# Kernel tuning notes

Measured on AMD Instinct MI355X. Metric: run time of the kernel, lower is better.

Reference implementation:

```python
import jax, jax.numpy as jnp
import numpy as np

N = 25000      # nodes
E = 400000     # edges (before self loops)
G = 64         # graphs in batch
H = 16         # attention heads
ITER = 10      # stacked main GATv2 layers


def setup_inputs():
    key = jax.random.key(0)
    c = [0]
    def nk():
        c[0] += 1
        return jax.random.fold_in(key, c[0])
    def glorot(shape):
        fan = shape[-2] + shape[-1]
        return jax.random.normal(nk(), shape, jnp.float32) * np.float32(np.sqrt(2.0 / fan))
    inp = {
        "x": jax.random.normal(nk(), (N, 2), jnp.float32),
        "edge_attr": jax.random.normal(nk(), (E, 2), jnp.float32),
        "edge_index": jax.random.randint(nk(), (2, E), 0, N, jnp.int32),
        "mask": jax.random.randint(nk(), (N,), 0, 2, jnp.int32),
        "batch": jnp.sort(jax.random.randint(nk(), (N,), 0, G, jnp.int32)),
        # gcn: GATv2Conv(2, 4, heads=16, edge_dim=2), concat -> 64
        "g0_Wl": glorot((2, 64)), "g0_bl": jnp.zeros((64,), jnp.float32),
        "g0_Wr": glorot((2, 64)), "g0_br": jnp.zeros((64,), jnp.float32),
        "g0_We": glorot((2, 64)), "g0_att": glorot((H, 4)),
        "g0_bias": jnp.zeros((64,), jnp.float32),
        "bn_gamma": jnp.ones((64,), jnp.float32),
        "bn_beta": jnp.zeros((64,), jnp.float32),
        "m_Wl": glorot((ITER, 64, 64)), "m_bl": jnp.zeros((ITER, 64), jnp.float32),
        "m_Wr": glorot((ITER, 64, 64)), "m_br": jnp.zeros((ITER, 64), jnp.float32),
        "m_We": glorot((ITER, 2, 64)), "m_att": glorot((ITER, H, 4)),
        "m_bias": jnp.zeros((ITER, 64), jnp.float32),
        # final: GATv2Conv(64, 1, heads=16, concat=False)
        "f_Wl": glorot((64, 16)), "f_bl": jnp.zeros((16,), jnp.float32),
        "f_Wr": glorot((64, 16)), "f_br": jnp.zeros((16,), jnp.float32),
        "f_We": glorot((2, 16)), "f_att": glorot((H, 1)),
        "f_bias": jnp.zeros((1,), jnp.float32),
        # sbs: GATv2Conv(64, 1, heads=16, concat=False)
        "s_Wl": glorot((64, 16)), "s_bl": jnp.zeros((16,), jnp.float32),
        "s_Wr": glorot((64, 16)), "s_br": jnp.zeros((16,), jnp.float32),
        "s_We": glorot((2, 16)), "s_att": glorot((H, 1)),
        "s_bias": jnp.zeros((1,), jnp.float32),
    }
    return inp


def _gatv2(x, src, dst, eattr, Wl, bl, Wr, br, We, att, bias, concat):
    """PyG GATv2Conv: x_l[j]+x_r[i]+e -> LeakyReLU(0.2) -> att dot -> segment softmax over dst."""
    n = x.shape[0]
    h, c = att.shape
    xl = (x @ Wl + bl).reshape(n, h, c)
    xr = (x @ Wr + br).reshape(n, h, c)
    e = (eattr @ We).reshape(-1, h, c)
    m = jax.nn.leaky_relu(xl[src] + xr[dst] + e, 0.2)          # [Etot,H,C]
    logit = jnp.einsum('ehc,hc->eh', m, att)                    # [Etot,H]
    lmax = jax.ops.segment_max(logit, dst, num_segments=n)
    ex = jnp.exp(logit - lmax[dst])
    den = jax.ops.segment_sum(ex, dst, num_segments=n)
    alpha = ex / den[dst]
    out = jax.ops.segment_sum(xl[src] * alpha[..., None], dst, num_segments=n)  # [N,H,C]
    out = out.reshape(n, h * c) if concat else out.mean(axis=1)
    return out + bias


def reference(x, edge_attr, edge_index, mask, batch,
              g0_Wl, g0_bl, g0_Wr, g0_br, g0_We, g0_att, g0_bias,
              bn_gamma, bn_beta,
              m_Wl, m_bl, m_Wr, m_br, m_We, m_att, m_bias,
              f_Wl, f_bl, f_Wr, f_br, f_We, f_att, f_bias,
              s_Wl, s_bl, s_Wr, s_br, s_We, s_att, s_bias):
    n = x.shape[0]
    src, dst = edge_index[0], edge_index[1]
    # add self loops; self-loop edge attr = mean of incoming edge attrs (fill_value='mean')
    ones = jnp.ones((src.shape[0],), jnp.float32)
    cnt = jax.ops.segment_sum(ones, dst, num_segments=n)
    esum = jax.ops.segment_sum(edge_attr, dst, num_segments=n)
    loop_attr = esum / jnp.maximum(cnt, 1.0)[:, None]
    arng = jnp.arange(n, dtype=edge_index.dtype)
    src2 = jnp.concatenate([src, arng])
    dst2 = jnp.concatenate([dst, arng])
    ea2 = jnp.concatenate([edge_attr, loop_attr], axis=0)

    h0 = _gatv2(x, src2, dst2, ea2, g0_Wl, g0_bl, g0_Wr, g0_br, g0_We, g0_att, g0_bias, True)
    mu = h0.mean(axis=0)
    var = h0.var(axis=0)
    h = jax.nn.leaky_relu((h0 - mu) * jax.lax.rsqrt(var + 1e-5) * bn_gamma + bn_beta, 0.01)

    def step(hc, p):
        Wl, bl, Wr, br, We, att, bias = p
        hc = jax.nn.leaky_relu(_gatv2(hc, src2, dst2, ea2, Wl, bl, Wr, br, We, att, bias, True), 0.01)
        return hc, None
    h, _ = jax.lax.scan(step, h, (m_Wl, m_bl, m_Wr, m_br, m_We, m_att, m_bias))

    mus = _gatv2(h, src2, dst2, ea2, s_Wl, s_bl, s_Wr, s_br, s_We, s_att, s_bias, False)[:, 0]  # [N]
    fin = _gatv2(h, src2, dst2, ea2, f_Wl, f_bl, f_Wr, f_br, f_We, f_att, f_bias, False)        # [N,1]
    w = (mask == 0).astype(jnp.float32)
    sums = jax.ops.segment_sum(fin * w[:, None], batch, num_segments=G)
    cnts = jax.ops.segment_sum(w, batch, num_segments=G)
    sat = (sums / jnp.maximum(cnts, 1.0)[:, None])[:, 0]  # [G]
    return mus, sat
```

## Files before the change

### kernel.cpp

```cpp
#include <hip/hip_runtime.h>


static __device__ __forceinline__ float lrelu(float x, float s) {
    return fmaxf(x, s * x);
}

__global__ void k_build0(const int* __restrict__ dst, int* __restrict__ cnt,
                         int* __restrict__ rank, int E) {
    int idx = blockIdx.x * blockDim.x + threadIdx.x;
    if (idx < E) rank[idx] = atomicAdd(&cnt[dst[idx]], 1);
}

__global__ void k_segoff(const int* __restrict__ cnt, int* __restrict__ row_start,
                         int* __restrict__ cursor, int n) {
    int i = blockIdx.x * blockDim.x + threadIdx.x;
    int lane = threadIdx.x & 63;
    int v = (i < n) ? cnt[i] : 0;
    int s = v;
#pragma unroll
    for (int off = 1; off < 64; off <<= 1) {
        int t = __shfl_up(s, off);
        if (lane >= off) s += t;
    }
    int wavetot = __shfl(s, 63);
    int base = 0;
    if (lane == 63) base = atomicAdd(cursor, wavetot);
    base = __shfl(base, 63);
    if (i < n) row_start[i] = base + s - v;
}

__global__ void k_scatter(const int* __restrict__ src, const int* __restrict__ dst,
                          const float* __restrict__ ea, const int* __restrict__ rank,
                          const int* __restrict__ row_start,
                          int* __restrict__ csr_src, float* __restrict__ csr_ea, int E) {
    int e = blockIdx.x * blockDim.x + threadIdx.x;
    if (e >= E) return;
    int pos = row_start[dst[e]] + rank[e];
    csr_src[pos] = src[e];
    *(float2*)(csr_ea + 2 * (size_t)pos) = *(const float2*)(ea + 2 * (size_t)e);
}

__launch_bounds__(256, 8)
__global__ void k_gat0(const float* __restrict__ x,
                       const int* __restrict__ row_start, const int* __restrict__ cnt,
                       const int* __restrict__ csr_src, const float* __restrict__ csr_ea,
                       const float* __restrict__ Wl, const float* __restrict__ bl,
                       const float* __restrict__ Wr, const float* __restrict__ br,
                       const float* __restrict__ We, const float* __restrict__ att,
                       const float* __restrict__ bias,
                       float* __restrict__ out, int n) {
    int d = (blockIdx.x * blockDim.x + threadIdx.x) >> 6;
    int lane = threadIdx.x & 63;
    if (d >= n) return;
    const int p0 = __builtin_amdgcn_readfirstlane(row_start[d]);
    const int deg = __builtin_amdgcn_readfirstlane(cnt[d]);
    const int p1 = p0 + deg;
    const float wl0 = Wl[lane], wl1 = Wl[64 + lane], blv = bl[lane];
    const float we0 = We[lane], we1 = We[64 + lane];
    const float av = att[lane];
    const float2 xd = *(const float2*)(x + 2 * (size_t)d);
    const float xrv = fmaf(xd.x, Wr[lane], fmaf(xd.y, Wr[64 + lane], br[lane]));

    float den0 = 0.f, acc0 = 0.f;
    float den1 = 0.f, acc1 = 0.f;
    float s0 = 0.f, s1 = 0.f;

    auto step = [&](float xv, float2 ea, bool valid, float& den, float& acc) {
        float vm = valid ? 1.f : 0.f;
        s0 = fmaf(vm, ea.x, s0);
        s1 = fmaf(vm, ea.y, s1);
        float tv = lrelu(xv + xrv + ea.x * we0 + ea.y * we1, 0.2f) * av;
        tv += __shfl_xor(tv, 1);
        tv += __shfl_xor(tv, 2);
        if (!valid) tv = -__builtin_inff();
        float w = __expf(tv);
        den += w;
        acc += w * xv;
    };

    for (int p = p0; p < p1; p += 4) {
        int q1 = min(p + 1, p1 - 1), q2 = min(p + 2, p1 - 1), q3 = min(p + 3, p1 - 1);
        int e0s = csr_src[p], e1s = csr_src[q1], e2s = csr_src[q2], e3s = csr_src[q3];
        float2 ea0 = *(const float2*)(csr_ea + 2 * (size_t)p);
        float2 ea1 = *(const float2*)(csr_ea + 2 * (size_t)q1);
        float2 ea2 = *(const float2*)(csr_ea + 2 * (size_t)q2);
        float2 ea3 = *(const float2*)(csr_ea + 2 * (size_t)q3);
        float2 xs0 = *(const float2*)(x + 2 * (size_t)e0s);
        float2 xs1 = *(const float2*)(x + 2 * (size_t)e1s);
        float2 xs2 = *(const float2*)(x + 2 * (size_t)e2s);
        float2 xs3 = *(const float2*)(x + 2 * (size_t)e3s);
        float xv0 = fmaf(xs0.x, wl0, fmaf(xs0.y, wl1, blv));
        float xv1 = fmaf(xs1.x, wl0, fmaf(xs1.y, wl1, blv));
        float xv2 = fmaf(xs2.x, wl0, fmaf(xs2.y, wl1, blv));
        float xv3 = fmaf(xs3.x, wl0, fmaf(xs3.y, wl1, blv));
        step(xv0, ea0, true, den0, acc0);
        step(xv1, ea1, p + 1 < p1, den1, acc1);
        step(xv2, ea2, p + 2 < p1, den0, acc0);
        step(xv3, ea3, p + 3 < p1, den1, acc1);
    }
    {
        float c = fmaxf((float)deg, 1.f);
        float se0 = s0 / c, se1 = s1 / c;
        float xv = fmaf(xd.x, wl0, fmaf(xd.y, wl1, blv));
        float tv = lrelu(xv + xrv + se0 * we0 + se1 * we1, 0.2f) * av;
        tv += __shfl_xor(tv, 1);
        tv += __shfl_xor(tv, 2);
        float w = __expf(tv);
        den0 += w;
        acc0 += w * xv;
    }
    out[((size_t)d << 6) + lane] = (acc0 + acc1) / (den0 + den1) + bias[lane];
}

__launch_bounds__(256)
__global__ void k_proj64(const float* __restrict__ h,
                         const float* __restrict__ Wl, const float* __restrict__ bl,
                         const float* __restrict__ Wr, const float* __restrict__ br,
                         const double* __restrict__ stats,
                         const float* __restrict__ bng, const float* __restrict__ bnb,
                         float* __restrict__ xl, float* __restrict__ xr, int n) {
    __shared__ float wsl[4096], wsr[4096], bna[64], bnbb[64];
    int t = threadIdx.x;
    for (int i = t; i < 4096; i += 256) { wsl[i] = Wl[i]; wsr[i] = Wr[i]; }
    if (t < 64) {
        double mu = stats[t] / n;
        double var = stats[64 + t] / n - mu * mu;
        float rs = (float)(1.0 / sqrt(var + 1e-5));
        float a = rs * bng[t];
        bna[t] = a;
        bnbb[t] = bnb[t] - (float)mu * a;
    }
    __syncthreads();
    int rg = t >> 2, cg4 = (t & 3) << 4;
    int r0 = blockIdx.x * 128 + rg * 2;
    float accl[2][16], accr[2][16];
#pragma unroll
    for (int r = 0; r < 2; ++r)
#pragma unroll
        for (int j = 0; j < 16; ++j) { accl[r][j] = 0.f; accr[r][j] = 0.f; }
    for (int k0 = 0; k0 < 64; k0 += 4) {
        float hk[2][4];
#pragma unroll
        for (int r = 0; r < 2; ++r) {
            int gr = r0 + r;
            float4 v = (gr < n) ? *(const float4*)(h + (size_t)gr * 64 + k0)
                                : make_float4(0.f, 0.f, 0.f, 0.f);
            hk[r][0] = v.x; hk[r][1] = v.y; hk[r][2] = v.z; hk[r][3] = v.w;
#pragma unroll
            for (int kk = 0; kk < 4; ++kk)
                hk[r][kk] = lrelu(hk[r][kk] * bna[k0 + kk] + bnbb[k0 + kk], 0.01f);
        }
#pragma unroll
        for (int kk = 0; kk < 4; ++kk) {
            const float* wl = wsl + (k0 + kk) * 64 + cg4;
            const float* wr = wsr + (k0 + kk) * 64 + cg4;
#pragma unroll
            for (int r = 0; r < 2; ++r)
#pragma unroll
                for (int j = 0; j < 16; ++j) {
                    accl[r][j] += hk[r][kk] * wl[j];
                    accr[r][j] += hk[r][kk] * wr[j];
                }
        }
    }
#pragma unroll
    for (int r = 0; r < 2; ++r) {
        int gr = r0 + r;
        if (gr < n) {
            float* ol = xl + (size_t)gr * 64 + cg4;
            float* orr = xr + (size_t)gr * 64 + cg4;
#pragma unroll
            for (int j = 0; j < 16; ++j) {
                ol[j] = accl[r][j] + bl[cg4 + j];
                orr[j] = accr[r][j] + br[cg4 + j];
            }
        }
    }
}

__device__ __forceinline__ float gat_node(const float* __restrict__ xl,
                                          const float* __restrict__ xr,
                                          const int* __restrict__ row_start,
                                          const int* __restrict__ cnt,
                                          const int* __restrict__ csr_src,
                                          const float* __restrict__ csr_ea,
                                          const float* __restrict__ We,
                                          const float* __restrict__ att,
                                          const float* __restrict__ bias,
                                          int d, int lane, int relu) {
    const int p0 = __builtin_amdgcn_readfirstlane(row_start[d]);
    const int deg = __builtin_amdgcn_readfirstlane(cnt[d]);
    const int p1 = p0 + deg;
    const float we0 = We[lane], we1 = We[64 + lane];
    const float av = att[lane];
    const float xrv = xr[((size_t)d << 6) + lane];

    float den0 = 0.f, acc0 = 0.f;
    float den1 = 0.f, acc1 = 0.f;
    float s0 = 0.f, s1 = 0.f;

    auto step = [&](float xv, float2 ea, bool valid, float& den, float& acc) {
        float vm = valid ? 1.f : 0.f;
        s0 = fmaf(vm, ea.x, s0);
        s1 = fmaf(vm, ea.y, s1);
        float tv = lrelu(xv + xrv + ea.x * we0 + ea.y * we1, 0.2f) * av;
        tv += __shfl_xor(tv, 1);
        tv += __shfl_xor(tv, 2);
        if (!valid) tv = -__builtin_inff();
        float w = __expf(tv);
        den += w;
        acc += w * xv;
    };

    for (int p = p0; p < p1; p += 4) {
        int q1 = min(p + 1, p1 - 1), q2 = min(p + 2, p1 - 1), q3 = min(p + 3, p1 - 1);
        int e0s = csr_src[p], e1s = csr_src[q1], e2s = csr_src[q2], e3s = csr_src[q3];
        float2 e0 = *(const float2*)(csr_ea + 2 * (size_t)p);
        float2 e1 = *(const float2*)(csr_ea + 2 * (size_t)q1);
        float2 e2 = *(const float2*)(csr_ea + 2 * (size_t)q2);
        float2 e3 = *(const float2*)(csr_ea + 2 * (size_t)q3);
        float x0 = xl[((size_t)e0s << 6) + lane];
        float x1 = xl[((size_t)e1s << 6) + lane];
        float x2 = xl[((size_t)e2s << 6) + lane];
        float x3 = xl[((size_t)e3s << 6) + lane];
        step(x0, e0, true, den0, acc0);
        step(x1, e1, p + 1 < p1, den1, acc1);
        step(x2, e2, p + 2 < p1, den0, acc0);
        step(x3, e3, p + 3 < p1, den1, acc1);
    }
    {
        float c = fmaxf((float)deg, 1.f);
        float se0 = s0 / c, se1 = s1 / c;
        float xv = xl[((size_t)d << 6) + lane];
        float tv = lrelu(xv + xrv + se0 * we0 + se1 * we1, 0.2f) * av;
        tv += __shfl_xor(tv, 1);
        tv += __shfl_xor(tv, 2);
        float w = __expf(tv);
        den0 += w;
        acc0 += w * xv;
    }
    float o = (acc0 + acc1) / (den0 + den1) + bias[lane];
    if (relu) o = lrelu(o, 0.01f);
    return o;
}

__launch_bounds__(64, 8)
__global__ void k_gat_proj2(const float* __restrict__ xl, const float* __restrict__ xr,
                            const int* __restrict__ row_start, const int* __restrict__ cnt,
                            const int* __restrict__ csr_src, const float* __restrict__ csr_ea,
                            const float* __restrict__ We, const float* __restrict__ att,
                            const float* __restrict__ bias,
                            const float* __restrict__ Wnl, const float* __restrict__ bnl,
                            const float* __restrict__ Wnr, const float* __restrict__ bnr,
                            float* __restrict__ xl_out, float* __restrict__ xr_out, int n) {
    int wave = blockIdx.x;
    int lane = threadIdx.x & 63;
    int d0 = wave * 2, d1 = d0 + 1;
    if (d0 >= n) return;
    float o0 = gat_node(xl, xr, row_start, cnt, csr_src, csr_ea, We, att, bias, d0, lane, 1);
    float o1 = (d1 < n)
                   ? gat_node(xl, xr, row_start, cnt, csr_src, csr_ea, We, att, bias, d1, lane, 1)
                   : 0.f;
    float al0a = 0.f, al0b = 0.f, ar0a = 0.f, ar0b = 0.f;
    float al1a = 0.f, al1b = 0.f, ar1a = 0.f, ar1b = 0.f;
#pragma unroll 4
    for (int k = 0; k < 64; k += 2) {
        float h0a = __shfl(o0, k), h0b = __shfl(o0, k + 1);
        float h1a = __shfl(o1, k), h1b = __shfl(o1, k + 1);
        float wl0 = Wnl[k * 64 + lane], wl1 = Wnl[(k + 1) * 64 + lane];
        float wr0 = Wnr[k * 64 + lane], wr1 = Wnr[(k + 1) * 64 + lane];
        al0a += h0a * wl0; al0b += h0b * wl1;
        ar0a += h0a * wr0; ar0b += h0b * wr1;
        al1a += h1a * wl0; al1b += h1b * wl1;
        ar1a += h1a * wr0; ar1b += h1b * wr1;
    }
    float bL = bnl[lane], bR = bnr[lane];
    xl_out[((size_t)d0 << 6) + lane] = al0a + al0b + bL;
    xr_out[((size_t)d0 << 6) + lane] = ar0a + ar0b + bR;
    if (d1 < n) {
        xl_out[((size_t)d1 << 6) + lane] = al1a + al1b + bL;
        xr_out[((size_t)d1 << 6) + lane] = ar1a + ar1b + bR;
    }
}

__launch_bounds__(64, 8)
__global__ void k_gat_projfin2(const float* __restrict__ xl, const float* __restrict__ xr,
                               const int* __restrict__ row_start, const int* __restrict__ cnt,
                               const int* __restrict__ csr_src, const float* __restrict__ csr_ea,
                               const float* __restrict__ We, const float* __restrict__ att,
                               const float* __restrict__ bias,
                               const float* __restrict__ fWl, const float* __restrict__ fbl,
                               const float* __restrict__ fWr, const float* __restrict__ fbr,
                               const float* __restrict__ sWl, const float* __restrict__ sbl,
                               const float* __restrict__ sWr, const float* __restrict__ sbr,
                               float* __restrict__ packed, int n) {
    int wave = blockIdx.x;
    int lane = threadIdx.x & 63;
    int d0 = wave * 2, d1 = d0 + 1;
    if (d0 >= n) return;
    float o0 = gat_node(xl, xr, row_start, cnt, csr_src, csr_ea, We, att, bias, d0, lane, 1);
    float o1 = (d1 < n)
                   ? gat_node(xl, xr, row_start, cnt, csr_src, csr_ea, We, att, bias, d1, lane, 1)
                   : 0.f;
    int q = lane >> 4, cc = lane & 15;
    const float* W = (q == 0) ? fWl : (q == 1) ? sWl : (q == 2) ? fWr : sWr;
    const float* B = (q == 0) ? fbl : (q == 1) ? sbl : (q == 2) ? fbr : sbr;
    float a0 = 0.f, a1 = 0.f, b0 = 0.f, b1 = 0.f;
#pragma unroll 4
    for (int k = 0; k < 64; k += 2) {
        float w0 = W[k * 16 + cc], w1 = W[(k + 1) * 16 + cc];
        a0 += __shfl(o0, k) * w0;
        a1 += __shfl(o0, k + 1) * w1;
        b0 += __shfl(o1, k) * w0;
        b1 += __shfl(o1, k + 1) * w1;
    }
    float bb = B[cc];
    packed[((size_t)d0 << 6) + lane] = a0 + a1 + bb;
    if (d1 < n) packed[((size_t)d1 << 6) + lane] = b0 + b1 + bb;
}

__launch_bounds__(256)
__global__ void k_gat_final(const float* __restrict__ packed,
                            const int* __restrict__ row_start, const int* __restrict__ cnt,
                            const int* __restrict__ csr_src, const float* __restrict__ csr_ea,
                            const float* __restrict__ fWe, const float* __restrict__ sWe,
                            const float* __restrict__ fatt, const float* __restrict__ satt,
                            const float* __restrict__ fbias, const float* __restrict__ sbias,
                            float* __restrict__ fin, float* __restrict__ mus, int n) {
    int hw = (blockIdx.x * blockDim.x + threadIdx.x) >> 5;
    if (hw >= n) return;
    int l = threadIdx.x & 31;
    int hh = l & 15, sel = l >> 4;
    const int d = hw;
    const int p0 = row_start[d], deg = cnt[d], p1 = p0 + deg;
    const float* We = sel ? sWe : fWe;
    float we0 = We[hh], we1 = We[16 + hh];
    float av = (sel ? satt : fatt)[hh];
    float xrv = packed[(size_t)d * 64 + 32 + sel * 16 + hh];
    int xli = sel * 16 + hh;

    float den0 = 0.f, acc0 = 0.f;
    float den1 = 0.f, acc1 = 0.f;
    float s0 = 0.f, s1 = 0.f;

    auto step = [&](float xv, float2 ea, bool valid, float& den, float& acc) {
        float vm = valid ? 1.f : 0.f;
        s0 = fmaf(vm, ea.x, s0);
        s1 = fmaf(vm, ea.y, s1);
        float t = lrelu(xv + xrv + ea.x * we0 + ea.y * we1, 0.2f) * av;
        if (!valid) t = -__builtin_inff();
        float w = __expf(t);
        den += w;
        acc += w * xv;
    };

    for (int p = p0; p < p1; p += 4) {
        int q1 = min(p + 1, p1 - 1), q2 = min(p + 2, p1 - 1), q3 = min(p + 3, p1 - 1);
        int e0s = csr_src[p], e1s = csr_src[q1], e2s = csr_src[q2], e3s = csr_src[q3];
        float2 e0 = *(const float2*)(csr_ea + 2 * (size_t)p);
        float2 e1 = *(const float2*)(csr_ea + 2 * (size_t)q1);
        float2 e2 = *(const float2*)(csr_ea + 2 * (size_t)q2);
        float2 e3 = *(const float2*)(csr_ea + 2 * (size_t)q3);
        float x0 = packed[(size_t)e0s * 64 + xli];
        float x1 = packed[(size_t)e1s * 64 + xli];
        float x2 = packed[(size_t)e2s * 64 + xli];
        float x3 = packed[(size_t)e3s * 64 + xli];
        step(x0, e0, true, den0, acc0);
        step(x1, e1, p + 1 < p1, den1, acc1);
        step(x2, e2, p + 2 < p1, den0, acc0);
        step(x3, e3, p + 3 < p1, den1, acc1);
    }
    {
        float c = fmaxf((float)deg, 1.f);
        float se0 = s0 / c, se1 = s1 / c;
        float xv = packed[(size_t)d * 64 + xli];
        float t = lrelu(xv + xrv + se0 * we0 + se1 * we1, 0.2f) * av;
        float w = __expf(t);
        den0 += w;
        acc0 += w * xv;
    }
    float val = (acc0 + acc1) / (den0 + den1);
#pragma unroll
    for (int w = 1; w < 16; w <<= 1) val += __shfl_xor(val, w);
    if ((threadIdx.x & 15) == 0) {
        float o = val * (1.f / 16.f) + (sel ? sbias[0] : fbias[0]);
        if (sel) mus[d] = o; else fin[d] = o;
    }
}


__global__ void k_bnstats(const float* __restrict__ h, double* __restrict__ stats, int n) {
    int c = threadIdx.x & 63;
    int s0 = blockIdx.x * (blockDim.x >> 6) + (threadIdx.x >> 6);
    int ns = gridDim.x * (blockDim.x >> 6);
    double s = 0.0, s2 = 0.0;
    for (int i = s0; i < n; i += ns) {
        float v = h[(size_t)i * 64 + c];
        s += v;
        s2 += (double)v * v;
    }
    atomicAdd(&stats[c], s);
    atomicAdd(&stats[64 + c], s2);
}


__global__ void k_sat_acc(const float* __restrict__ fin, const int* __restrict__ mask,
                          const int* __restrict__ batch,
                          float* __restrict__ sums, float* __restrict__ cnts, int n) {
    int i = blockIdx.x * blockDim.x + threadIdx.x;
    int lane = threadIdx.x & 63;
    int g = (i < n) ? batch[i] : -1;
    float c = (i < n && mask[i] == 0) ? 1.f : 0.f;
    float v = (c > 0.f) ? fin[i] : 0.f;
#pragma unroll
    for (int off = 1; off < 64; off <<= 1) {
        float v2 = __shfl_down(v, off);
        float c2 = __shfl_down(c, off);
        int g2 = __shfl_down(g, off);
        if (lane + off < 64 && g2 == g) { v += v2; c += c2; }
    }
    int gprev = __shfl_up(g, 1);
    bool head = (lane == 0) || (gprev != g);
    if (head && g >= 0 && c > 0.f) {
        atomicAdd(&sums[g], v);
        atomicAdd(&cnts[g], c);
    }
}

__global__ void k_sat_fin(const float* __restrict__ sums, const float* __restrict__ cnts,
                          float* __restrict__ out, int g) {
    int i = threadIdx.x;
    if (i < g) out[i] = sums[i] / fmaxf(cnts[i], 1.f);
}


extern "C" void kernel_launch(void* const* d_in, const int* in_sizes, int n_in,
                              void* d_out, int out_size, void* d_ws, size_t ws_size,
                              hipStream_t stream) {
    const float* x = (const float*)d_in[0];
    const float* eat = (const float*)d_in[1];
    const int* ei = (const int*)d_in[2];
    const int* mask = (const int*)d_in[3];
    const int* batch = (const int*)d_in[4];
    const float* g0_Wl = (const float*)d_in[5];
    const float* g0_bl = (const float*)d_in[6];
    const float* g0_Wr = (const float*)d_in[7];
    const float* g0_br = (const float*)d_in[8];
    const float* g0_We = (const float*)d_in[9];
    const float* g0_att = (const float*)d_in[10];
    const float* g0_bias = (const float*)d_in[11];
    const float* bn_g = (const float*)d_in[12];
    const float* bn_b = (const float*)d_in[13];
    const float* m_Wl = (const float*)d_in[14];
    const float* m_bl = (const float*)d_in[15];
    const float* m_Wr = (const float*)d_in[16];
    const float* m_br = (const float*)d_in[17];
    const float* m_We = (const float*)d_in[18];
    const float* m_att = (const float*)d_in[19];
    const float* m_bias = (const float*)d_in[20];
    const float* f_Wl = (const float*)d_in[21];
    const float* f_bl = (const float*)d_in[22];
    const float* f_Wr = (const float*)d_in[23];
    const float* f_br = (const float*)d_in[24];
    const float* f_We = (const float*)d_in[25];
    const float* f_att = (const float*)d_in[26];
    const float* f_bias = (const float*)d_in[27];
    const float* s_Wl = (const float*)d_in[28];
    const float* s_bl = (const float*)d_in[29];
    const float* s_Wr = (const float*)d_in[30];
    const float* s_br = (const float*)d_in[31];
    const float* s_We = (const float*)d_in[32];
    const float* s_att = (const float*)d_in[33];
    const float* s_bias = (const float*)d_in[34];

    const int N = in_sizes[3];
    const int E = in_sizes[1] / 2;
    const int G = out_size - N;
    const int ITER = in_sizes[14] / 4096;
    const int* srcp = ei;
    const int* dstp = ei + E;

    char* wsb = (char*)d_ws;
    size_t off = 0;
    auto alloc = [&](size_t b) { void* p = wsb + off; off = (off + b + 255) & ~(size_t)255; return p; };
    int* cnt = (int*)alloc((size_t)N * 4);
    int* cursor = (int*)alloc(256);
    double* stats = (double*)alloc(128 * 8);
    float* sums = (float*)alloc((size_t)G * 4);
    float* cnts = (float*)alloc((size_t)G * 4);
    size_t zero_bytes = off;
    int* rank = (int*)alloc((size_t)E * 4);
    int* row_start = (int*)alloc((size_t)N * 4);
    int* csr_src = (int*)alloc((size_t)(E + 4) * 4);
    float* csr_ea = (float*)alloc((size_t)(E + 4) * 8);
    float* xlA = (float*)alloc((size_t)N * 256);
    float* xrA = (float*)alloc((size_t)N * 256);
    float* xlB = (float*)alloc((size_t)N * 256);
    float* xrB = (float*)alloc((size_t)N * 256);
    float* hbuf = (float*)alloc((size_t)N * 256);
    float* fin = (float*)alloc((size_t)N * 4);
    (void)ws_size; (void)n_in;

    float* outv = (float*)d_out;

    hipMemsetAsync(d_ws, 0, zero_bytes, stream);
    const int tb = 256;
    const int ggrid = (N * 64 + 255) / 256;
    const int npair = (N + 1) / 2;
    k_build0<<<(E + tb - 1) / tb, tb, 0, stream>>>(dstp, cnt, rank, E);
    k_segoff<<<(N + tb - 1) / tb, tb, 0, stream>>>(cnt, row_start, cursor, N);
    k_scatter<<<(E + tb - 1) / tb, tb, 0, stream>>>(srcp, dstp, eat, rank, row_start,
                                                    csr_src, csr_ea, E);

    k_gat0<<<ggrid, tb, 0, stream>>>(x, row_start, cnt, csr_src, csr_ea,
                                     g0_Wl, g0_bl, g0_Wr, g0_br,
                                     g0_We, g0_att, g0_bias, hbuf, N);
    k_bnstats<<<128, 256, 0, stream>>>(hbuf, stats, N);
    k_proj64<<<(N + 127) / 128, 256, 0, stream>>>(hbuf, m_Wl, m_bl, m_Wr, m_br,
                                                  stats, bn_g, bn_b, xlA, xrA, N);

    float* cur_l = xlA; float* cur_r = xrA;
    float* alt_l = xlB; float* alt_r = xrB;
    for (int l = 0; l < ITER; ++l) {
        if (l < ITER - 1) {
            k_gat_proj2<<<npair, 64, 0, stream>>>(cur_l, cur_r, row_start, cnt, csr_src, csr_ea,
                                                  m_We + l * 128, m_att + l * 64, m_bias + l * 64,
                                                  m_Wl + (size_t)(l + 1) * 4096, m_bl + (l + 1) * 64,
                                                  m_Wr + (size_t)(l + 1) * 4096, m_br + (l + 1) * 64,
                                                  alt_l, alt_r, N);
        } else {
            k_gat_projfin2<<<npair, 64, 0, stream>>>(cur_l, cur_r, row_start, cnt, csr_src, csr_ea,
                                                     m_We + l * 128, m_att + l * 64, m_bias + l * 64,
                                                     f_Wl, f_bl, f_Wr, f_br,
                                                     s_Wl, s_bl, s_Wr, s_br,
                                                     alt_l, N);
        }
        float* t;
        t = cur_l; cur_l = alt_l; alt_l = t;
        t = cur_r; cur_r = alt_r; alt_r = t;
    }
    k_gat_final<<<(N * 32 + tb - 1) / tb, tb, 0, stream>>>(cur_l, row_start, cnt, csr_src, csr_ea,
                                                           f_We, s_We, f_att, s_att,
                                                           f_bias, s_bias, fin, outv, N);
    k_sat_acc<<<(N + tb - 1) / tb, tb, 0, stream>>>(fin, mask, batch, sums, cnts, N);
    k_sat_fin<<<1, 64, 0, stream>>>(sums, cnts, outv + N, G);
}
```

Measured before the change: 627.3 us.

## Split fused GAT aggregation and projection into separate kernels with LDS-tiled GEMM

Unfuses each main layer into a pure aggregation kernel (256-thread blocks, two nodes per wave, writing h to a buffer) and a separate projection kernel that stages the 64x64 weights in shared memory and computes a register-tiled 2x16 output per thread. The old fused path read weights from global memory per wave and used many shuffles. The new path removes that cost and lets the aggregation run at higher occupancy. In exchange it adds an extra write and read of the N x 64 hidden state plus an extra kernel launch per layer.

```diff
diff --git a/kernel.cpp b/kernel.cpp
--- a/kernel.cpp
+++ b/kernel.cpp
@@ -244,79 +244,133 @@
     return o;
 }
 
-__launch_bounds__(64, 8)
-__global__ void k_gat_proj2(const float* __restrict__ xl, const float* __restrict__ xr,
-                            const int* __restrict__ row_start, const int* __restrict__ cnt,
-                            const int* __restrict__ csr_src, const float* __restrict__ csr_ea,
-                            const float* __restrict__ We, const float* __restrict__ att,
-                            const float* __restrict__ bias,
-                            const float* __restrict__ Wnl, const float* __restrict__ bnl,
-                            const float* __restrict__ Wnr, const float* __restrict__ bnr,
-                            float* __restrict__ xl_out, float* __restrict__ xr_out, int n) {
-    int wave = blockIdx.x;
+__launch_bounds__(256, 8)
+__global__ void k_gat2e(const float* __restrict__ xl, const float* __restrict__ xr,
+                        const int* __restrict__ row_start, const int* __restrict__ cnt,
+                        const int* __restrict__ csr_src, const float* __restrict__ csr_ea,
+                        const float* __restrict__ We, const float* __restrict__ att,
+                        const float* __restrict__ bias,
+                        float* __restrict__ out, int n) {
+    int wave = (blockIdx.x * blockDim.x + threadIdx.x) >> 6;
     int lane = threadIdx.x & 63;
-    int d0 = wave * 2, d1 = d0 + 1;
+    int d0 = wave * 2;
     if (d0 >= n) return;
     float o0 = gat_node(xl, xr, row_start, cnt, csr_src, csr_ea, We, att, bias, d0, lane, 1);
-    float o1 = (d1 < n)
-                   ? gat_node(xl, xr, row_start, cnt, csr_src, csr_ea, We, att, bias, d1, lane, 1)
-                   : 0.f;
-    float al0a = 0.f, al0b = 0.f, ar0a = 0.f, ar0b = 0.f;
-    float al1a = 0.f, al1b = 0.f, ar1a = 0.f, ar1b = 0.f;
-#pragma unroll 4
-    for (int k = 0; k < 64; k += 2) {
-        float h0a = __shfl(o0, k), h0b = __shfl(o0, k + 1);
-        float h1a = __shfl(o1, k), h1b = __shfl(o1, k + 1);
-        float wl0 = Wnl[k * 64 + lane], wl1 = Wnl[(k + 1) * 64 + lane];
-        float wr0 = Wnr[k * 64 + lane], wr1 = Wnr[(k + 1) * 64 + lane];
-        al0a += h0a * wl0; al0b += h0b * wl1;
-        ar0a += h0a * wr0; ar0b += h0b * wr1;
-        al1a += h1a * wl0; al1b += h1b * wl1;
-        ar1a += h1a * wr0; ar1b += h1b * wr1;
-    }
-    float bL = bnl[lane], bR = bnr[lane];
-    xl_out[((size_t)d0 << 6) + lane] = al0a + al0b + bL;
-    xr_out[((size_t)d0 << 6) + lane] = ar0a + ar0b + bR;
+    out[((size_t)d0 << 6) + lane] = o0;
+    int d1 = d0 + 1;
     if (d1 < n) {
-        xl_out[((size_t)d1 << 6) + lane] = al1a + al1b + bL;
-        xr_out[((size_t)d1 << 6) + lane] = ar1a + ar1b + bR;
-    }
-}
-
-__launch_bounds__(64, 8)
-__global__ void k_gat_projfin2(const float* __restrict__ xl, const float* __restrict__ xr,
-                               const int* __restrict__ row_start, const int* __restrict__ cnt,
-                               const int* __restrict__ csr_src, const float* __restrict__ csr_ea,
-                               const float* __restrict__ We, const float* __restrict__ att,
-                               const float* __restrict__ bias,
-                               const float* __restrict__ fWl, const float* __restrict__ fbl,
-                               const float* __restrict__ fWr, const float* __restrict__ fbr,
-                               const float* __restrict__ sWl, const float* __restrict__ sbl,
-                               const float* __restrict__ sWr, const float* __restrict__ sbr,
-                               float* __restrict__ packed, int n) {
-    int wave = blockIdx.x;
-    int lane = threadIdx.x & 63;
-    int d0 = wave * 2, d1 = d0 + 1;
-    if (d0 >= n) return;
-    float o0 = gat_node(xl, xr, row_start, cnt, csr_src, csr_ea, We, att, bias, d0, lane, 1);
-    float o1 = (d1 < n)
-                   ? gat_node(xl, xr, row_start, cnt, csr_src, csr_ea, We, att, bias, d1, lane, 1)
-                   : 0.f;
-    int q = lane >> 4, cc = lane & 15;
-    const float* W = (q == 0) ? fWl : (q == 1) ? sWl : (q == 2) ? fWr : sWr;
-    const float* B = (q == 0) ? fbl : (q == 1) ? sbl : (q == 2) ? fbr : sbr;
-    float a0 = 0.f, a1 = 0.f, b0 = 0.f, b1 = 0.f;
-#pragma unroll 4
-    for (int k = 0; k < 64; k += 2) {
-        float w0 = W[k * 16 + cc], w1 = W[(k + 1) * 16 + cc];
-        a0 += __shfl(o0, k) * w0;
-        a1 += __shfl(o0, k + 1) * w1;
-        b0 += __shfl(o1, k) * w0;
-        b1 += __shfl(o1, k + 1) * w1;
-    }
-    float bb = B[cc];
-    packed[((size_t)d0 << 6) + lane] = a0 + a1 + bb;
-    if (d1 < n) packed[((size_t)d1 << 6) + lane] = b0 + b1 + bb;
+        float o1 = gat_node(xl, xr, row_start, cnt, csr_src, csr_ea, We, att, bias, d1, lane, 1);
+        out[((size_t)d1 << 6) + lane] = o1;
+    }
+}
+
+__launch_bounds__(256)
+__global__ void k_projdual(const float* __restrict__ h,
+                           const float* __restrict__ Wl, const float* __restrict__ bl,
+                           const float* __restrict__ Wr, const float* __restrict__ br,
+                           float* __restrict__ xl, float* __restrict__ xr, int n) {
+    __shared__ float wsl[4096], wsr[4096];
+    int t = threadIdx.x;
+    for (int i = t; i < 4096; i += 256) { wsl[i] = Wl[i]; wsr[i] = Wr[i]; }
+    __syncthreads();
+    int rg = t >> 2, cg4 = (t & 3) << 4;
+    int r0 = blockIdx.x * 128 + rg * 2;
+    float accl[2][16], accr[2][16];
+#pragma unroll
+    for (int r = 0; r < 2; ++r)
+#pragma unroll
+        for (int j = 0; j < 16; ++j) { accl[r][j] = 0.f; accr[r][j] = 0.f; }
+    for (int k0 = 0; k0 < 64; k0 += 4) {
+        float hk[2][4];
+#pragma unroll
+        for (int r = 0; r < 2; ++r) {
+            int gr = r0 + r;
+            float4 v = (gr < n) ? *(const float4*)(h + (size_t)gr * 64 + k0)
+                                : make_float4(0.f, 0.f, 0.f, 0.f);
+            hk[r][0] = v.x; hk[r][1] = v.y; hk[r][2] = v.z; hk[r][3] = v.w;
+        }
+#pragma unroll
+        for (int kk = 0; kk < 4; ++kk) {
+            const float* wl = wsl + (k0 + kk) * 64 + cg4;
+            const float* wr = wsr + (k0 + kk) * 64 + cg4;
+#pragma unroll
+            for (int r = 0; r < 2; ++r)
+#pragma unroll
+                for (int j = 0; j < 16; ++j) {
+                    accl[r][j] += hk[r][kk] * wl[j];
+                    accr[r][j] += hk[r][kk] * wr[j];
+                }
+        }
+    }
+#pragma unroll
+    for (int r = 0; r < 2; ++r) {
+        int gr = r0 + r;
+        if (gr < n) {
+            float* ol = xl + (size_t)gr * 64 + cg4;
+            float* orr = xr + (size_t)gr * 64 + cg4;
+#pragma unroll
+            for (int j = 0; j < 16; ++j) {
+                ol[j] = accl[r][j] + bl[cg4 + j];
+                orr[j] = accr[r][j] + br[cg4 + j];
+            }
+        }
+    }
+}
+
+__launch_bounds__(256)
+__global__ void k_projpk(const float* __restrict__ h,
+                         const float* __restrict__ fWl, const float* __restrict__ fbl,
+                         const float* __restrict__ sWl, const float* __restrict__ sbl,
+                         const float* __restrict__ fWr, const float* __restrict__ fbr,
+                         const float* __restrict__ sWr, const float* __restrict__ sbr,
+                         float* __restrict__ packed, int n) {
+    __shared__ float ws[4096], bs[64];
+    int t = threadIdx.x;
+    for (int i = t; i < 4096; i += 256) {
+        int k = i >> 6, c = i & 63, q = c >> 4, cc = c & 15;
+        const float* W = (q == 0) ? fWl : (q == 1) ? sWl : (q == 2) ? fWr : sWr;
+        ws[i] = W[k * 16 + cc];
+    }
+    if (t < 64) {
+        int q = t >> 4, cc = t & 15;
+        const float* B = (q == 0) ? fbl : (q == 1) ? sbl : (q == 2) ? fbr : sbr;
+        bs[t] = B[cc];
+    }
+    __syncthreads();
+    int rg = t >> 2, cg4 = (t & 3) << 4;
+    int r0 = blockIdx.x * 128 + rg * 2;
+    float acc[2][16];
+#pragma unroll
+    for (int r = 0; r < 2; ++r)
+#pragma unroll
+        for (int j = 0; j < 16; ++j) acc[r][j] = 0.f;
+    for (int k0 = 0; k0 < 64; k0 += 4) {
+        float hk[2][4];
+#pragma unroll
+        for (int r = 0; r < 2; ++r) {
+            int gr = r0 + r;
+            float4 v = (gr < n) ? *(const float4*)(h + (size_t)gr * 64 + k0)
+                                : make_float4(0.f, 0.f, 0.f, 0.f);
+            hk[r][0] = v.x; hk[r][1] = v.y; hk[r][2] = v.z; hk[r][3] = v.w;
+        }
+#pragma unroll
+        for (int kk = 0; kk < 4; ++kk) {
+            const float* w = ws + (k0 + kk) * 64 + cg4;
+#pragma unroll
+            for (int r = 0; r < 2; ++r)
+#pragma unroll
+                for (int j = 0; j < 16; ++j) acc[r][j] += hk[r][kk] * w[j];
+        }
+    }
+#pragma unroll
+    for (int r = 0; r < 2; ++r) {
+        int gr = r0 + r;
+        if (gr < n) {
+            float* op = packed + (size_t)gr * 64 + cg4;
+#pragma unroll
+            for (int j = 0; j < 16; ++j) op[j] = acc[r][j] + bs[cg4 + j];
+        }
+    }
 }
 
 __launch_bounds__(256)
@@ -507,6 +561,8 @@
     const int tb = 256;
     const int ggrid = (N * 64 + 255) / 256;
     const int npair = (N + 1) / 2;
+    const int ggrid2 = (npair * 64 + 255) / 256;
+    const int pgrid = (N + 127) / 128;
     k_build0<<<(E + tb - 1) / tb, tb, 0, stream>>>(dstp, cnt, rank, E);
     k_segoff<<<(N + tb - 1) / tb, tb, 0, stream>>>(cnt, row_start, cursor, N);
     k_scatter<<<(E + tb - 1) / tb, tb, 0, stream>>>(srcp, dstp, eat, rank, row_start,
@@ -516,24 +572,25 @@
                                      g0_Wl, g0_bl, g0_Wr, g0_br,
                                      g0_We, g0_att, g0_bias, hbuf, N);
     k_bnstats<<<128, 256, 0, stream>>>(hbuf, stats, N);
-    k_proj64<<<(N + 127) / 128, 256, 0, stream>>>(hbuf, m_Wl, m_bl, m_Wr, m_br,
-                                                  stats, bn_g, bn_b, xlA, xrA, N);
+    k_proj64<<<pgrid, 256, 0, stream>>>(hbuf, m_Wl, m_bl, m_Wr, m_br,
+                                        stats, bn_g, bn_b, xlA, xrA, N);
 
     float* cur_l = xlA; float* cur_r = xrA;
     float* alt_l = xlB; float* alt_r = xrB;
     for (int l = 0; l < ITER; ++l) {
+        k_gat2e<<<ggrid2, tb, 0, stream>>>(cur_l, cur_r, row_start, cnt, csr_src, csr_ea,
+                                           m_We + l * 128, m_att + l * 64, m_bias + l * 64,
+                                           hbuf, N);
         if (l < ITER - 1) {
-            k_gat_proj2<<<npair, 64, 0, stream>>>(cur_l, cur_r, row_start, cnt, csr_src, csr_ea,
-                                                  m_We + l * 128, m_att + l * 64, m_bias + l * 64,
+            k_projdual<<<pgrid, 256, 0, stream>>>(hbuf,
                                                   m_Wl + (size_t)(l + 1) * 4096, m_bl + (l + 1) * 64,
                                                   m_Wr + (size_t)(l + 1) * 4096, m_br + (l + 1) * 64,
                                                   alt_l, alt_r, N);
         } else {
-            k_gat_projfin2<<<npair, 64, 0, stream>>>(cur_l, cur_r, row_start, cnt, csr_src, csr_ea,
-                                                     m_We + l * 128, m_att + l * 64, m_bias + l * 64,
-                                                     f_Wl, f_bl, f_Wr, f_br,
-                                                     s_Wl, s_bl, s_Wr, s_br,
-                                                     alt_l, N);
+            k_projpk<<<pgrid, 256, 0, stream>>>(hbuf,
+                                                f_Wl, f_bl, s_Wl, s_bl,
+                                                f_Wr, f_br, s_Wr, s_br,
+                                                alt_l, N);
         }
         float* t;
         t = cur_l; cur_l = alt_l; alt_l = t;
```

After: 693.2 us. 1.11x slower.
